# Kernel optimization log

Hardware: AMD Instinct MI355X
Metric: run time of the kernel (lower is better)

## Reference

```python
import jax, jax.numpy as jnp
import numpy as np

B, N, G = 8, 262144, 64
EPS = 1e-6


def _log_transform(x):
    return jnp.sign(x) * jnp.log1p(jnp.abs(x))


def _group_mean_depth(points, valid, groups):
    # points: (B,N,3), valid: (B,N) bool, groups: (B,N) int in [0,G)
    z = points[..., 2]
    w = valid.astype(z.dtype)
    seg = (groups.astype(jnp.int32) + jnp.arange(B, dtype=jnp.int32)[:, None] * G).ravel()
    sums = jax.ops.segment_sum((z * w).ravel(), seg, num_segments=B * G)
    cnts = jax.ops.segment_sum(w.ravel(), seg, num_segments=B * G)
    mean = jnp.where(cnts > 0, sums / jnp.maximum(cnts, 1.0), 1.0)  # empty group -> 1.0 (skipped in torch loop)
    safe = jnp.maximum(jnp.abs(mean), EPS)
    per_point = safe[seg].reshape(z.shape)
    return jnp.where(valid, per_point, 1.0)


def _normalize_points(points, valid, groups):
    md = _group_mean_depth(points, valid, groups)
    return jnp.where(valid[..., None], points, 0.0) / md[..., None]


def _masked_mean(loss, valid):
    vm = valid if loss.ndim == valid.ndim else jnp.broadcast_to(valid[..., None], loss.shape)
    return jnp.where(vm, loss, 0.0).sum() / (vm.sum().astype(loss.dtype) + 1e-6)


def setup_inputs() -> dict:
    key = jax.random.key(0)
    ks = jax.random.split(key, 13)
    f = lambda k, s: jax.random.normal(k, s, dtype=jnp.float32)
    return {
        'pred_points': f(ks[0], (B, N, 3)),
        'target_points': f(ks[1], (B, N, 3)),
        'pred_2d': f(ks[2], (B, N, 2)),
        'target_2d': f(ks[3], (B, N, 2)),
        'pred_vis': f(ks[4], (B, N, 1)),
        'target_vis': jax.random.uniform(ks[5], (B, N), dtype=jnp.float32),
        'pred_disp': f(ks[6], (B, N, 3)),
        'target_disp': f(ks[7], (B, N, 3)),
        'pred_normal': f(ks[8], (B, N, 3)),
        'target_normal': f(ks[9], (B, N, 3)),
        'confidence': f(ks[10], (B, N, 1)),
        'mask': jax.random.randint(ks[11], (B, N), 0, 2, dtype=jnp.int32),
        'groups': jax.random.randint(ks[12], (B, N), 0, G, dtype=jnp.int32),
    }


def reference(pred_points, target_points, pred_2d, target_2d, pred_vis, target_vis,
              pred_disp, target_disp, pred_normal, target_normal, confidence, mask, groups):
    lambda_3d, lambda_raw_3d, lambda_2d = 1.0, 0.0, 0.1
    lambda_vis, lambda_disp, lambda_normal, lambda_conf = 0.1, 0.1, 0.5, 0.2
    valid = mask.astype(bool)

    # L_3D: per-group scale-invariant normalization + log transform + masked L1
    pn = _log_transform(_normalize_points(pred_points, valid, groups))
    tn = _log_transform(_normalize_points(target_points, valid, groups))
    l_3d = _masked_mean(jnp.abs(pn - tn), valid)

    # L_raw3D: raw camera-space L1 (weight 0 by default)
    l_raw3d = _masked_mean(jnp.abs(pred_points - target_points), valid)

    # L_2D
    l_2d = _masked_mean(jnp.abs(pred_2d - target_2d), valid)

    # L_vis: BCE with logits
    x = pred_vis[..., 0]
    bce = jnp.maximum(x, 0.0) - x * target_vis + jnp.log1p(jnp.exp(-jnp.abs(x)))
    l_vis = _masked_mean(bce, valid)

    # L_disp
    l_disp = _masked_mean(jnp.abs(pred_disp - target_disp), valid)

    # L_normal: 1 - cosine similarity of unit-normalized vectors
    def _unit(v):
        n = jnp.linalg.norm(v, axis=-1, keepdims=True)
        return v / jnp.maximum(n, 1e-12)
    cos = (_unit(pred_normal) * _unit(target_normal)).sum(-1)
    l_normal = _masked_mean(1.0 - cos, valid)

    # L_conf: Kendall penalty s = -log(c)
    l_conf = _masked_mean(confidence[..., 0], valid)

    return (lambda_3d * l_3d + lambda_raw_3d * l_raw3d + lambda_2d * l_2d
            + lambda_vis * l_vis + lambda_disp * l_disp
            + lambda_normal * l_normal + lambda_conf * l_conf)
```

## Files before the change

kernel.cpp:

```cpp
#include <hip/hip_runtime.h>
#include <math.h>

#define BB  8
#define NN  262144
#define GG  64
#define NBG (BB * GG)
#define TOT (BB * NN)
#define NBLK 2048

#define PART_F 4096
#define WS_ZERO_BYTES (3 * NBG * 4)

__device__ __forceinline__ float wredf(float v) {
#pragma unroll
    for (int o = 32; o > 0; o >>= 1) v += __shfl_down(v, o, 64);
    return v;
}

__global__ __launch_bounds__(256) void k_group(const float* __restrict__ pp,
                                               const float* __restrict__ tp,
                                               const int* __restrict__ mask,
                                               const int* __restrict__ grp,
                                               float* __restrict__ ws) {
    __shared__ float sP[GG], sT[GG], sC[GG];
    if (threadIdx.x < GG) { sP[threadIdx.x] = 0.f; sT[threadIdx.x] = 0.f; sC[threadIdx.x] = 0.f; }
    __syncthreads();

    const int base = blockIdx.x * 2048;
    const int b = base >> 18;
#pragma unroll
    for (int j = 0; j < 2048; j += 256) {
        int i = base + j + threadIdx.x;
        if (mask[i]) {
            int g = grp[i];
            atomicAdd(&sP[g], pp[i * 3 + 2]);
            atomicAdd(&sT[g], tp[i * 3 + 2]);
            atomicAdd(&sC[g], 1.0f);
        }
    }
    __syncthreads();
    if (threadIdx.x < GG) {
        float c = sC[threadIdx.x];
        if (c != 0.0f) {
            int e = b * GG + threadIdx.x;
            atomicAdd(&ws[e], sP[threadIdx.x]);
            atomicAdd(&ws[NBG + e], sT[threadIdx.x]);
            atomicAdd(&ws[2 * NBG + e], c);
        }
    }
}

__global__ __launch_bounds__(512) void k_groups_final(float* __restrict__ ws) {
    __shared__ float red[NBG];
    int j = threadIdx.x;
    float c = ws[2 * NBG + j];
    float mP = (c > 0.f) ? (ws[j] / fmaxf(c, 1.f)) : 1.0f;
    float mT = (c > 0.f) ? (ws[NBG + j] / fmaxf(c, 1.f)) : 1.0f;
    ws[3 * NBG + j] = 1.0f / fmaxf(fabsf(mP), 1e-6f);
    ws[4 * NBG + j] = 1.0f / fmaxf(fabsf(mT), 1e-6f);
    red[j] = c;
    __syncthreads();
    for (int s = 256; s > 0; s >>= 1) {
        if (j < s) red[j] += red[j + s];
        __syncthreads();
    }
    if (j == 0) ws[5 * NBG] = red[0];
}

__global__ __launch_bounds__(256) void k_loss(const float* __restrict__ pp,
                                              const float* __restrict__ tp,
                                              const float* __restrict__ p2,
                                              const float* __restrict__ t2,
                                              const float* __restrict__ pv,
                                              const float* __restrict__ tv,
                                              const float* __restrict__ pd,
                                              const float* __restrict__ td,
                                              const float* __restrict__ pn,
                                              const float* __restrict__ tn,
                                              const float* __restrict__ cf,
                                              const int* __restrict__ mask,
                                              const int* __restrict__ grp,
                                              float* __restrict__ ws) {
    const float* invP = ws + 3 * NBG;
    const float* invT = ws + 4 * NBG;

    float s3d = 0.f, s2 = 0.f, sv = 0.f, sd = 0.f, sn = 0.f, sc = 0.f;

    const int base = blockIdx.x * 1024;
#pragma unroll
    for (int j = 0; j < 1024; j += 256) {
        int i = base + j + threadIdx.x;
        float w = (float)mask[i];
        int e = ((i >> 18) << 6) | grp[i];
        float iP = invP[e], iT = invT[e];
        int i3 = i * 3;
        int i2 = i * 2;

        float t3 = 0.f;
#pragma unroll
        for (int k = 0; k < 3; k++) {
            float a = pp[i3 + k] * iP;
            float b2 = tp[i3 + k] * iT;
            float la = copysignf(log1pf(fabsf(a)), a);
            float lb = copysignf(log1pf(fabsf(b2)), b2);
            t3 += fabsf(la - lb);
        }
        s3d += w * t3;
        s2 += w * (fabsf(p2[i2] - t2[i2]) + fabsf(p2[i2 + 1] - t2[i2 + 1]));
        {
            float x = pv[i], t = tv[i];
            sv += w * (fmaxf(x, 0.f) - x * t + log1pf(expf(-fabsf(x))));
        }
        sd += w * (fabsf(pd[i3] - td[i3]) + fabsf(pd[i3 + 1] - td[i3 + 1]) + fabsf(pd[i3 + 2] - td[i3 + 2]));
        {
            float ax = pn[i3], ay = pn[i3 + 1], az = pn[i3 + 2];
            float bx = tn[i3], by = tn[i3 + 1], bz = tn[i3 + 2];
            float na = fmaxf(sqrtf(ax * ax + ay * ay + az * az), 1e-12f);
            float nb = fmaxf(sqrtf(bx * bx + by * by + bz * bz), 1e-12f);
            sn += w * (1.0f - (ax * bx + ay * by + az * bz) / (na * nb));
        }
        sc += w * cf[i];
    }

    __shared__ float sred[4][6];
    float vals[6] = {s3d, s2, sv, sd, sn, sc};
    int wid = threadIdx.x >> 6, lane = threadIdx.x & 63;
#pragma unroll
    for (int k = 0; k < 6; k++) {
        float r = wredf(vals[k]);
        if (lane == 0) sred[wid][k] = r;
    }
    __syncthreads();
    if (threadIdx.x < 6) {
        float t = sred[0][threadIdx.x] + sred[1][threadIdx.x]
                + sred[2][threadIdx.x] + sred[3][threadIdx.x];
        ws[PART_F + threadIdx.x * NBLK + blockIdx.x] = t;
    }
}

__global__ __launch_bounds__(256) void k_final(const float* __restrict__ ws,
                                               float* __restrict__ out) {
    const float* part = ws + PART_F;
    double loc[6] = {0, 0, 0, 0, 0, 0};
    for (int j = threadIdx.x; j < NBLK; j += 256) {
#pragma unroll
        for (int k = 0; k < 6; k++) loc[k] += (double)part[k * NBLK + j];
    }
    __shared__ double dred[4][6];
    int wid = threadIdx.x >> 6, lane = threadIdx.x & 63;
#pragma unroll
    for (int k = 0; k < 6; k++) {
        double v = loc[k];
#pragma unroll
        for (int o = 32; o > 0; o >>= 1) v += __shfl_down(v, o, 64);
        if (lane == 0) dred[wid][k] = v;
    }
    __syncthreads();
    if (threadIdx.x == 0) {
        double a[6];
#pragma unroll
        for (int k = 0; k < 6; k++)
            a[k] = dred[0][k] + dred[1][k] + dred[2][k] + dred[3][k];
        double nv = (double)ws[5 * NBG];
        double d1 = nv + 1e-6;
        double d3 = 3.0 * nv + 1e-6;
        double l3d   = a[0] / d3;
        double l2d   = a[1] / (2.0 * nv + 1e-6);
        double lvis  = a[2] / d1;
        double ldisp = a[3] / d3;
        double lnorm = a[4] / d1;
        double lconf = a[5] / d1;
        out[0] = (float)(l3d + 0.1 * (l2d + lvis + ldisp) + 0.5 * lnorm + 0.2 * lconf);
    }
}

extern "C" void kernel_launch(void* const* d_in, const int* in_sizes, int n_in,
                              void* d_out, int out_size, void* d_ws, size_t ws_size,
                              hipStream_t stream) {
    const float* pp = (const float*)d_in[0];
    const float* tp = (const float*)d_in[1];
    const float* p2 = (const float*)d_in[2];
    const float* t2 = (const float*)d_in[3];
    const float* pv = (const float*)d_in[4];
    const float* tv = (const float*)d_in[5];
    const float* pd = (const float*)d_in[6];
    const float* td = (const float*)d_in[7];
    const float* pn = (const float*)d_in[8];
    const float* tn = (const float*)d_in[9];
    const float* cf = (const float*)d_in[10];
    const int* mask = (const int*)d_in[11];
    const int* grp  = (const int*)d_in[12];
    float* ws = (float*)d_ws;
    float* out = (float*)d_out;

    hipMemsetAsync(d_ws, 0, WS_ZERO_BYTES, stream);
    k_group<<<TOT / 2048, 256, 0, stream>>>(pp, tp, mask, grp, ws);
    k_groups_final<<<1, NBG, 0, stream>>>(ws);
    k_loss<<<NBLK, 256, 0, stream>>>(pp, tp, p2, t2, pv, tv, pd, td, pn, tn, cf, mask, grp, ws);
    k_final<<<1, 256, 0, stream>>>(ws, out);
}
```

Before: 82.80 us.

## Vectorize loads, two points per thread, fast log/exp intrinsics, split group atomics

Both the group-sum and loss kernels now handle two consecutive points per thread and read them with int2/float2/float4 vector loads. Grids grow to 4096 blocks, and the group kernel spreads its global atomics over two copies split by block parity, which the finalize kernel sums back. The inverse-mean pairs are interleaved so one float2 load fetches both scales. Transcendentals switch to hardware exp2/log2 intrinsics and rsqrt, trading some accuracy (log1p of small values in particular) for fewer instructions.

```diff
diff --git a/kernel.cpp b/kernel.cpp
--- a/kernel.cpp
+++ b/kernel.cpp
@@ -4,12 +4,24 @@
 #define BB  8
 #define NN  262144
 #define GG  64
-#define NBG (BB * GG)
-#define TOT (BB * NN)
-#define NBLK 2048
-
-#define PART_F 4096
-#define WS_ZERO_BYTES (3 * NBG * 4)
+#define NBG 512
+#define TOT 2097152
+#define NBLK 4096
+
+#define ZP_F   0
+#define ZT_F   1024
+#define CNT_F  2048
+#define PAIR_F 3072
+#define NV_F   4096
+#define PART_F 4352
+#define WS_ZERO_BYTES (3072 * 4)
+
+#define LN2   0.6931471805599453f
+#define LOG2E 1.4426950408889634f
+
+__device__ __forceinline__ float fexp2(float x) { return __builtin_amdgcn_exp2f(x); }
+__device__ __forceinline__ float flog2(float x) { return __builtin_amdgcn_logf(x); }
+__device__ __forceinline__ float flog1p(float x) { return flog2(1.0f + x) * LN2; }
 
 __device__ __forceinline__ float wredf(float v) {
 #pragma unroll
@@ -26,26 +38,25 @@
     if (threadIdx.x < GG) { sP[threadIdx.x] = 0.f; sT[threadIdx.x] = 0.f; sC[threadIdx.x] = 0.f; }
     __syncthreads();
 
-    const int base = blockIdx.x * 2048;
-    const int b = base >> 18;
-#pragma unroll
-    for (int j = 0; j < 2048; j += 256) {
-        int i = base + j + threadIdx.x;
-        if (mask[i]) {
-            int g = grp[i];
-            atomicAdd(&sP[g], pp[i * 3 + 2]);
-            atomicAdd(&sT[g], tp[i * 3 + 2]);
-            atomicAdd(&sC[g], 1.0f);
-        }
-    }
+    const int t = blockIdx.x * 256 + threadIdx.x;
+    const int p0 = t << 1;
+    const int b = p0 >> 18;
+
+    const int2 M  = *(const int2*)(mask + p0);
+    const int2 Gp = *(const int2*)(grp + p0);
+    const float zP0 = pp[3 * p0 + 2], zP1 = pp[3 * p0 + 5];
+    const float zT0 = tp[3 * p0 + 2], zT1 = tp[3 * p0 + 5];
+
+    if (M.x) { atomicAdd(&sP[Gp.x], zP0); atomicAdd(&sT[Gp.x], zT0); atomicAdd(&sC[Gp.x], 1.f); }
+    if (M.y) { atomicAdd(&sP[Gp.y], zP1); atomicAdd(&sT[Gp.y], zT1); atomicAdd(&sC[Gp.y], 1.f); }
     __syncthreads();
     if (threadIdx.x < GG) {
         float c = sC[threadIdx.x];
         if (c != 0.0f) {
-            int e = b * GG + threadIdx.x;
-            atomicAdd(&ws[e], sP[threadIdx.x]);
-            atomicAdd(&ws[NBG + e], sT[threadIdx.x]);
-            atomicAdd(&ws[2 * NBG + e], c);
+            int e = (blockIdx.x & 1) * NBG + b * GG + threadIdx.x;
+            atomicAdd(&ws[ZP_F + e], sP[threadIdx.x]);
+            atomicAdd(&ws[ZT_F + e], sT[threadIdx.x]);
+            atomicAdd(&ws[CNT_F + e], c);
         }
     }
 }
@@ -53,18 +64,20 @@
 __global__ __launch_bounds__(512) void k_groups_final(float* __restrict__ ws) {
     __shared__ float red[NBG];
     int j = threadIdx.x;
-    float c = ws[2 * NBG + j];
-    float mP = (c > 0.f) ? (ws[j] / fmaxf(c, 1.f)) : 1.0f;
-    float mT = (c > 0.f) ? (ws[NBG + j] / fmaxf(c, 1.f)) : 1.0f;
-    ws[3 * NBG + j] = 1.0f / fmaxf(fabsf(mP), 1e-6f);
-    ws[4 * NBG + j] = 1.0f / fmaxf(fabsf(mT), 1e-6f);
+    float c  = ws[CNT_F + j] + ws[CNT_F + NBG + j];
+    float sp = ws[ZP_F + j]  + ws[ZP_F + NBG + j];
+    float st = ws[ZT_F + j]  + ws[ZT_F + NBG + j];
+    float mP = (c > 0.f) ? (sp / fmaxf(c, 1.f)) : 1.0f;
+    float mT = (c > 0.f) ? (st / fmaxf(c, 1.f)) : 1.0f;
+    ws[PAIR_F + 2 * j]     = 1.0f / fmaxf(fabsf(mP), 1e-6f);
+    ws[PAIR_F + 2 * j + 1] = 1.0f / fmaxf(fabsf(mT), 1e-6f);
     red[j] = c;
     __syncthreads();
     for (int s = 256; s > 0; s >>= 1) {
         if (j < s) red[j] += red[j + s];
         __syncthreads();
     }
-    if (j == 0) ws[5 * NBG] = red[0];
+    if (j == 0) ws[NV_F] = red[0];
 }
 
 __global__ __launch_bounds__(256) void k_loss(const float* __restrict__ pp,
@@ -81,45 +94,78 @@
                                               const int* __restrict__ mask,
                                               const int* __restrict__ grp,
                                               float* __restrict__ ws) {
-    const float* invP = ws + 3 * NBG;
-    const float* invT = ws + 4 * NBG;
-
-    float s3d = 0.f, s2 = 0.f, sv = 0.f, sd = 0.f, sn = 0.f, sc = 0.f;
-
-    const int base = blockIdx.x * 1024;
-#pragma unroll
-    for (int j = 0; j < 1024; j += 256) {
-        int i = base + j + threadIdx.x;
-        float w = (float)mask[i];
-        int e = ((i >> 18) << 6) | grp[i];
-        float iP = invP[e], iT = invT[e];
-        int i3 = i * 3;
-        int i2 = i * 2;
-
-        float t3 = 0.f;
-#pragma unroll
-        for (int k = 0; k < 3; k++) {
-            float a = pp[i3 + k] * iP;
-            float b2 = tp[i3 + k] * iT;
-            float la = copysignf(log1pf(fabsf(a)), a);
-            float lb = copysignf(log1pf(fabsf(b2)), b2);
-            t3 += fabsf(la - lb);
+    const float* pairs = ws + PAIR_F;
+
+    const int t = blockIdx.x * 256 + threadIdx.x;
+    const int p0 = t << 1;
+    const int bb6 = (p0 >> 18) << 6;
+
+    const int2 M  = *(const int2*)(mask + p0);
+    const int2 Gp = *(const int2*)(grp + p0);
+    const float w0 = (float)M.x, w1 = (float)M.y;
+    const float2 pr0 = *(const float2*)(pairs + 2 * (bb6 | Gp.x));
+    const float2 pr1 = *(const float2*)(pairs + 2 * (bb6 | Gp.y));
+
+    float s3d, s2, sv, sd, sn, sc;
+
+    {
+        const float2* A  = (const float2*)(pp + 3 * p0);
+        const float2* Bv = (const float2*)(tp + 3 * p0);
+        float P[6], T[6];
+        *(float2*)&P[0] = A[0];  *(float2*)&P[2] = A[1];  *(float2*)&P[4] = A[2];
+        *(float2*)&T[0] = Bv[0]; *(float2*)&T[2] = Bv[1]; *(float2*)&T[4] = Bv[2];
+        float a0 = 0.f, a1 = 0.f;
+#pragma unroll
+        for (int c = 0; c < 3; c++) {
+            float a = P[c] * pr0.x,     b = T[c] * pr0.y;
+            a0 += fabsf(copysignf(flog1p(fabsf(a)), a) - copysignf(flog1p(fabsf(b)), b));
+            float a2 = P[3 + c] * pr1.x, b2 = T[3 + c] * pr1.y;
+            a1 += fabsf(copysignf(flog1p(fabsf(a2)), a2) - copysignf(flog1p(fabsf(b2)), b2));
         }
-        s3d += w * t3;
-        s2 += w * (fabsf(p2[i2] - t2[i2]) + fabsf(p2[i2 + 1] - t2[i2 + 1]));
-        {
-            float x = pv[i], t = tv[i];
-            sv += w * (fmaxf(x, 0.f) - x * t + log1pf(expf(-fabsf(x))));
+        s3d = w0 * a0 + w1 * a1;
+    }
+    {
+        float4 A  = *(const float4*)(p2 + 2 * p0);
+        float4 Bv = *(const float4*)(t2 + 2 * p0);
+        s2 = w0 * (fabsf(A.x - Bv.x) + fabsf(A.y - Bv.y))
+           + w1 * (fabsf(A.z - Bv.z) + fabsf(A.w - Bv.w));
+    }
+    {
+        float2 X  = *(const float2*)(pv + p0);
+        float2 Tg = *(const float2*)(tv + p0);
+        float2 C  = *(const float2*)(cf + p0);
+        float soft0 = flog2(1.0f + fexp2(-fabsf(X.x) * LOG2E)) * LN2;
+        float soft1 = flog2(1.0f + fexp2(-fabsf(X.y) * LOG2E)) * LN2;
+        sv = w0 * (fmaxf(X.x, 0.f) - X.x * Tg.x + soft0)
+           + w1 * (fmaxf(X.y, 0.f) - X.y * Tg.y + soft1);
+        sc = w0 * C.x + w1 * C.y;
+    }
+    {
+        const float2* A  = (const float2*)(pd + 3 * p0);
+        const float2* Bv = (const float2*)(td + 3 * p0);
+        float P[6], T[6];
+        *(float2*)&P[0] = A[0];  *(float2*)&P[2] = A[1];  *(float2*)&P[4] = A[2];
+        *(float2*)&T[0] = Bv[0]; *(float2*)&T[2] = Bv[1]; *(float2*)&T[4] = Bv[2];
+        sd = w0 * (fabsf(P[0] - T[0]) + fabsf(P[1] - T[1]) + fabsf(P[2] - T[2]))
+           + w1 * (fabsf(P[3] - T[3]) + fabsf(P[4] - T[4]) + fabsf(P[5] - T[5]));
+    }
+    {
+        const float2* A  = (const float2*)(pn + 3 * p0);
+        const float2* Bv = (const float2*)(tn + 3 * p0);
+        float P[6], T[6];
+        *(float2*)&P[0] = A[0];  *(float2*)&P[2] = A[1];  *(float2*)&P[4] = A[2];
+        *(float2*)&T[0] = Bv[0]; *(float2*)&T[2] = Bv[1]; *(float2*)&T[4] = Bv[2];
+        sn = 0.f;
+#pragma unroll
+        for (int k = 0; k < 2; k++) {
+            float ax = P[3 * k], ay = P[3 * k + 1], az = P[3 * k + 2];
+            float bx = T[3 * k], by = T[3 * k + 1], bz = T[3 * k + 2];
+            float na = fmaf(ax, ax, fmaf(ay, ay, az * az));
+            float nb = fmaf(bx, bx, fmaf(by, by, bz * bz));
+            float dot = fmaf(ax, bx, fmaf(ay, by, az * bz));
+            float r = __frsqrt_rn(fmaxf(na, 1e-24f)) * __frsqrt_rn(fmaxf(nb, 1e-24f));
+            sn += (k ? w1 : w0) * (1.0f - dot * r);
         }
-        sd += w * (fabsf(pd[i3] - td[i3]) + fabsf(pd[i3 + 1] - td[i3 + 1]) + fabsf(pd[i3 + 2] - td[i3 + 2]));
-        {
-            float ax = pn[i3], ay = pn[i3 + 1], az = pn[i3 + 2];
-            float bx = tn[i3], by = tn[i3 + 1], bz = tn[i3 + 2];
-            float na = fmaxf(sqrtf(ax * ax + ay * ay + az * az), 1e-12f);
-            float nb = fmaxf(sqrtf(bx * bx + by * by + bz * bz), 1e-12f);
-            sn += w * (1.0f - (ax * bx + ay * by + az * bz) / (na * nb));
-        }
-        sc += w * cf[i];
     }
 
     __shared__ float sred[4][6];
@@ -132,9 +178,9 @@
     }
     __syncthreads();
     if (threadIdx.x < 6) {
-        float t = sred[0][threadIdx.x] + sred[1][threadIdx.x]
-                + sred[2][threadIdx.x] + sred[3][threadIdx.x];
-        ws[PART_F + threadIdx.x * NBLK + blockIdx.x] = t;
+        float tt = sred[0][threadIdx.x] + sred[1][threadIdx.x]
+                 + sred[2][threadIdx.x] + sred[3][threadIdx.x];
+        ws[PART_F + threadIdx.x * NBLK + blockIdx.x] = tt;
     }
 }
 
@@ -161,7 +207,7 @@
 #pragma unroll
         for (int k = 0; k < 6; k++)
             a[k] = dred[0][k] + dred[1][k] + dred[2][k] + dred[3][k];
-        double nv = (double)ws[5 * NBG];
+        double nv = (double)ws[NV_F];
         double d1 = nv + 1e-6;
         double d3 = 3.0 * nv + 1e-6;
         double l3d   = a[0] / d3;
@@ -193,8 +239,8 @@
     float* ws = (float*)d_ws;
     float* out = (float*)d_out;
 
-    hipMemsetAsync(d_ws, 0, WS_ZERO_BYTES, stream);
-    k_group<<<TOT / 2048, 256, 0, stream>>>(pp, tp, mask, grp, ws);
+    (void)hipMemsetAsync(d_ws, 0, WS_ZERO_BYTES, stream);
+    k_group<<<NBLK, 256, 0, stream>>>(pp, tp, mask, grp, ws);
     k_groups_final<<<1, NBG, 0, stream>>>(ws);
     k_loss<<<NBLK, 256, 0, stream>>>(pp, tp, p2, t2, pv, tv, pd, td, pn, tn, cf, mask, grp, ws);
     k_final<<<1, 256, 0, stream>>>(ws, out);
```

Measured after the change: 86.31 us. +4.2%, slower.
